# Kernel optimization log

Hardware: AMD Instinct MI355X
Metric: run time of the kernel (lower is better)

The kernel has to match this reference:

```python
import jax, jax.numpy as jnp
import numpy as np

N = 20000
E = 320000
D = 512
H = 512


def _gcn_norm(edge_index, num_nodes):
    # PyG GCNConv: add self-loops, then sym-normalize with in-degree of A+I
    src = jnp.concatenate([edge_index[0], jnp.arange(num_nodes)])
    dst = jnp.concatenate([edge_index[1], jnp.arange(num_nodes)])
    deg = jax.ops.segment_sum(jnp.ones_like(dst, dtype=jnp.float32), dst, num_segments=num_nodes)
    dinv = jnp.where(deg > 0, jax.lax.rsqrt(deg), 0.0)
    norm = dinv[src] * dinv[dst]  # [E+N]
    return src, dst, norm


def _gcn_layer(x, src, dst, norm, W, b, num_nodes):
    h = x @ W                          # [N, out]
    msg = h[src] * norm[:, None]       # gather + scale, [E+N, out]
    out = jax.ops.segment_sum(msg, dst, num_segments=num_nodes)  # scatter-add
    return out + b


def setup_inputs() -> dict:
    key = jax.random.key(0)
    ks = jax.random.split(key, 8)
    features = jax.random.normal(ks[0], (N, D), dtype=jnp.float32)
    edge_index = jax.random.randint(ks[1], (2, E), 0, N, dtype=jnp.int64)
    edge_attr = jax.random.normal(ks[2], (E, 1), dtype=jnp.float32)  # unused by GCNConv
    s1 = 1.0 / np.sqrt(D)
    s2 = 1.0 / np.sqrt(H)
    W1 = jax.random.uniform(ks[3], (D, H), dtype=jnp.float32, minval=-s1, maxval=s1)
    b1 = jnp.zeros((H,), dtype=jnp.float32)
    W2 = jax.random.uniform(ks[4], (H, H), dtype=jnp.float32, minval=-s2, maxval=s2)
    b2 = jnp.zeros((H,), dtype=jnp.float32)
    return {"features": features, "edge_index": edge_index, "edge_attr": edge_attr,
            "W1": W1, "b1": b1, "W2": W2, "b2": b2}


def reference(features, edge_index, edge_attr, W1, b1, W2, b2):
    src, dst, norm = _gcn_norm(edge_index, N)
    x = jax.nn.relu(_gcn_layer(features, src, dst, norm, W1, b1, N))
    x = jax.nn.relu(_gcn_layer(x, src, dst, norm, W2, b2, N))
    # global_max_pool over the single graph (batch = all zeros) -> [1, H]
    return jnp.max(x, axis=0, keepdims=True)
```

## Files before the change

kernel.cpp:

```cpp
#include <hip/hip_runtime.h>

#define N_NODES 20000
#define MP      20096
#define N_EDGES 320000
#define DIM     512
#define SCAN_BLOCKS 79
#define MAXP_BLOCKS 256
#define MAXP_ROWS   79

typedef _Float16 half8 __attribute__((ext_vector_type(8)));
typedef _Float16 half4v __attribute__((ext_vector_type(4)));
typedef float floatx4 __attribute__((ext_vector_type(4)));

#define GLD16(g, l) __builtin_amdgcn_global_load_lds( \
    (const __attribute__((address_space(1))) unsigned int*)(g), \
    (__attribute__((address_space(3))) unsigned int*)(l), 16, 0, 0)

__global__ void k_init(int* __restrict__ cnt, float* __restrict__ out) {
    int i = blockIdx.x * blockDim.x + threadIdx.x;
    if (i < N_NODES) cnt[i] = 0;
    if (i < DIM) out[i] = 0.f;
}

__global__ void k_count(const int* __restrict__ dst, int* __restrict__ cnt) {
    int e = blockIdx.x * blockDim.x + threadIdx.x;
    if (e < N_EDGES) atomicAdd(&cnt[dst[e]], 1);
}

__global__ __launch_bounds__(256) void k_scan_a(const int* __restrict__ cnt,
                                                int* __restrict__ bsum) {
    __shared__ int buf[256];
    int gi = blockIdx.x * 256 + threadIdx.x;
    buf[threadIdx.x] = (gi < N_NODES) ? cnt[gi] : 0;
    __syncthreads();
    for (int off = 128; off > 0; off >>= 1) {
        if (threadIdx.x < off) buf[threadIdx.x] += buf[threadIdx.x + off];
        __syncthreads();
    }
    if (threadIdx.x == 0) bsum[blockIdx.x] = buf[0];
}

__global__ __launch_bounds__(128) void k_scan_b(const int* __restrict__ bsum,
                                                int* __restrict__ bbase) {
    __shared__ int buf[128];
    int tid = threadIdx.x;
    int v = (tid < SCAN_BLOCKS) ? bsum[tid] : 0;
    buf[tid] = v;
    __syncthreads();
    for (int off = 1; off < 128; off <<= 1) {
        int t = (tid >= off) ? buf[tid - off] : 0;
        __syncthreads();
        buf[tid] += t;
        __syncthreads();
    }
    if (tid < SCAN_BLOCKS) bbase[tid] = buf[tid] - v;
}

__global__ __launch_bounds__(256) void k_scan_c(const int* __restrict__ cnt,
                                                const int* __restrict__ bbase,
                                                int* __restrict__ offs,
                                                int* __restrict__ cursor,
                                                float* __restrict__ dinv) {
    __shared__ int buf[256];
    int tid = threadIdx.x;
    int gi = blockIdx.x * 256 + tid;
    int v = (gi < N_NODES) ? cnt[gi] : 0;
    buf[tid] = v;
    __syncthreads();
    for (int off = 1; off < 256; off <<= 1) {
        int t = (tid >= off) ? buf[tid - off] : 0;
        __syncthreads();
        buf[tid] += t;
        __syncthreads();
    }
    int base = bbase[blockIdx.x];
    if (gi < N_NODES) {
        int incl = base + buf[tid];
        offs[gi + 1] = incl;
        cursor[gi] = incl - v;
        dinv[gi] = rsqrtf((float)v + 1.0f);
        if (gi == 0) offs[0] = 0;
    } else if (gi < MP) {
        dinv[gi] = 0.f;
    }
}

__global__ void k_fill(const int* __restrict__ src, const int* __restrict__ dst,
                       int* __restrict__ cursor, int* __restrict__ csr_src) {
    int e = blockIdx.x * blockDim.x + threadIdx.x;
    if (e < N_EDGES) {
        int d = dst[e];
        int pos = atomicAdd(&cursor[d], 1);
        csr_src[pos] = src[e];
    }
}

__global__ __launch_bounds__(256) void k_cvt_feat(const float* __restrict__ F,
                                                  _Float16* __restrict__ A) {
    int i = blockIdx.x * blockDim.x + threadIdx.x;
    int e = i * 4;
    int row = e >> 9;
    half4v o;
    if (row < N_NODES) {
        float4 v = *(const float4*)&F[e];
        o[0] = (_Float16)v.x; o[1] = (_Float16)v.y;
        o[2] = (_Float16)v.z; o[3] = (_Float16)v.w;
    } else {
        o[0] = o[1] = o[2] = o[3] = (_Float16)0.f;
    }
    *(half4v*)&A[e] = o;
}

__global__ __launch_bounds__(256) void k_cvt_w(const float* __restrict__ W1,
                                               const float* __restrict__ W2,
                                               _Float16* __restrict__ Wt1,
                                               _Float16* __restrict__ Wt2) {
    const float* W = blockIdx.z ? W2 : W1;
    _Float16* Wt = blockIdx.z ? Wt2 : Wt1;
    __shared__ float tile[32][33];
    int bx = blockIdx.x * 32, by = blockIdx.y * 32;
    int x = threadIdx.x & 31, y4 = (threadIdx.x >> 5) * 4;
#pragma unroll
    for (int r = 0; r < 4; ++r)
        tile[y4 + r][x] = W[(size_t)(by + y4 + r) * DIM + bx + x];
    __syncthreads();
#pragma unroll
    for (int r = 0; r < 4; ++r)
        Wt[(size_t)(bx + y4 + r) * DIM + by + x] = (_Float16)tile[x][y4 + r];
}

__global__ __launch_bounds__(256) void k_gemm_f16(const _Float16* __restrict__ A,
                                                  const _Float16* __restrict__ Bt,
                                                  const float* __restrict__ dinv,
                                                  _Float16* __restrict__ G) {
    __shared__ _Float16 As[128 * 32];
    __shared__ _Float16 Bs[128 * 32];

    int t = threadIdx.x;
    int w = t >> 6, lane = t & 63;
    int lm = lane & 15, quad = lane >> 4;
    int m0 = blockIdx.x * 128, n0 = blockIdx.y * 128;
    int wm = (w & 1) * 64, wn = (w >> 1) * 64;

    floatx4 acc[4][4];
#pragma unroll
    for (int i = 0; i < 4; ++i)
#pragma unroll
        for (int j = 0; j < 4; ++j) acc[i][j] = (floatx4){0.f, 0.f, 0.f, 0.f};

    for (int k0 = 0; k0 < DIM; k0 += 32) {
        __syncthreads();
#pragma unroll
        for (int i = 0; i < 2; ++i) {
            int s = i * 256 + t;
            int m = s >> 2, kk = (s & 3) * 8;
            GLD16(A + (size_t)(m0 + m) * DIM + k0 + kk, As + s * 8);
            GLD16(Bt + (size_t)(n0 + m) * DIM + k0 + kk, Bs + s * 8);
        }
        __syncthreads();

        half8 af[4], bf[4];
#pragma unroll
        for (int i = 0; i < 4; ++i)
            af[i] = *(const half8*)&As[(wm + i * 16 + lm) * 32 + quad * 8];
#pragma unroll
        for (int j = 0; j < 4; ++j)
            bf[j] = *(const half8*)&Bs[(wn + j * 16 + lm) * 32 + quad * 8];
#pragma unroll
        for (int i = 0; i < 4; ++i)
#pragma unroll
            for (int j = 0; j < 4; ++j)
                acc[i][j] = __builtin_amdgcn_mfma_f32_16x16x32_f16(af[i], bf[j], acc[i][j], 0, 0, 0);
    }

#pragma unroll
    for (int i = 0; i < 4; ++i)
#pragma unroll
        for (int r = 0; r < 4; ++r) {
            int row = m0 + wm + i * 16 + quad * 4 + r;
            float dd = dinv[row];
#pragma unroll
            for (int j = 0; j < 4; ++j) {
                int col = n0 + wn + j * 16 + lm;
                G[(size_t)row * DIM + col] = (_Float16)(dd * acc[i][j][r]);
            }
        }
}

__global__ __launch_bounds__(256) void k_agg(const _Float16* __restrict__ g,
                                             const float* __restrict__ dinv,
                                             const int* __restrict__ offs,
                                             const int* __restrict__ csr_src,
                                             const float* __restrict__ bias,
                                             _Float16* __restrict__ out, int nNodesOut) {
    int node = blockIdx.x * 4 + (threadIdx.x >> 6);
    int lane = threadIdx.x & 63;
    int f0 = lane * 8;
    if (node >= nNodesOut) return;
    if (node >= N_NODES) {
        half8 z;
#pragma unroll
        for (int i = 0; i < 8; ++i) z[i] = (_Float16)0.f;
        *(half8*)&out[(size_t)node * DIM + f0] = z;
        return;
    }
    float acc[8];
    half8 self = *(const half8*)&g[(size_t)node * DIM + f0];
#pragma unroll
    for (int i = 0; i < 8; ++i) acc[i] = (float)self[i];

    int beg = offs[node], end = offs[node + 1];
    int e = beg;
    for (; e + 8 <= end; e += 8) {
        int s0 = csr_src[e],     s1 = csr_src[e + 1], s2 = csr_src[e + 2], s3 = csr_src[e + 3];
        int s4 = csr_src[e + 4], s5 = csr_src[e + 5], s6 = csr_src[e + 6], s7 = csr_src[e + 7];
        half8 v0 = *(const half8*)&g[(size_t)s0 * DIM + f0];
        half8 v1 = *(const half8*)&g[(size_t)s1 * DIM + f0];
        half8 v2 = *(const half8*)&g[(size_t)s2 * DIM + f0];
        half8 v3 = *(const half8*)&g[(size_t)s3 * DIM + f0];
        half8 v4 = *(const half8*)&g[(size_t)s4 * DIM + f0];
        half8 v5 = *(const half8*)&g[(size_t)s5 * DIM + f0];
        half8 v6 = *(const half8*)&g[(size_t)s6 * DIM + f0];
        half8 v7 = *(const half8*)&g[(size_t)s7 * DIM + f0];
#pragma unroll
        for (int i = 0; i < 8; ++i)
            acc[i] += ((float)v0[i] + (float)v1[i]) + ((float)v2[i] + (float)v3[i]) +
                      ((float)v4[i] + (float)v5[i]) + ((float)v6[i] + (float)v7[i]);
    }
    for (; e + 4 <= end; e += 4) {
        int s0 = csr_src[e], s1 = csr_src[e + 1], s2 = csr_src[e + 2], s3 = csr_src[e + 3];
        half8 v0 = *(const half8*)&g[(size_t)s0 * DIM + f0];
        half8 v1 = *(const half8*)&g[(size_t)s1 * DIM + f0];
        half8 v2 = *(const half8*)&g[(size_t)s2 * DIM + f0];
        half8 v3 = *(const half8*)&g[(size_t)s3 * DIM + f0];
#pragma unroll
        for (int i = 0; i < 8; ++i)
            acc[i] += ((float)v0[i] + (float)v1[i]) + ((float)v2[i] + (float)v3[i]);
    }
    for (; e < end; ++e) {
        int s = csr_src[e];
        half8 v = *(const half8*)&g[(size_t)s * DIM + f0];
#pragma unroll
        for (int i = 0; i < 8; ++i) acc[i] += (float)v[i];
    }
    float dd = dinv[node];
    float4 b0 = *(const float4*)&bias[f0];
    float4 b1 = *(const float4*)&bias[f0 + 4];
    float bb[8] = {b0.x, b0.y, b0.z, b0.w, b1.x, b1.y, b1.z, b1.w};
    half8 o;
#pragma unroll
    for (int i = 0; i < 8; ++i) o[i] = (_Float16)fmaxf(fmaf(dd, acc[i], bb[i]), 0.f);
    *(half8*)&out[(size_t)node * DIM + f0] = o;
}

__global__ __launch_bounds__(256) void k_maxpool(const _Float16* __restrict__ x,
                                                 float* __restrict__ out) {
    __shared__ float lmax[4][DIM];
    int stream = threadIdx.x >> 6, lane = threadIdx.x & 63;
    int f0 = lane * 8;
    int r0 = blockIdx.x * MAXP_ROWS;
    int r1 = min(r0 + MAXP_ROWS, N_NODES);

    float m[8];
#pragma unroll
    for (int i = 0; i < 8; ++i) m[i] = 0.f;
    for (int r = r0 + stream; r < r1; r += 4) {
        half8 v = *(const half8*)&x[(size_t)r * DIM + f0];
#pragma unroll
        for (int i = 0; i < 8; ++i) m[i] = fmaxf(m[i], (float)v[i]);
    }
#pragma unroll
    for (int i = 0; i < 8; ++i) lmax[stream][f0 + i] = m[i];
    __syncthreads();
#pragma unroll
    for (int rep = 0; rep < 2; ++rep) {
        int f = rep * 256 + threadIdx.x;
        float v = fmaxf(fmaxf(lmax[0][f], lmax[1][f]), fmaxf(lmax[2][f], lmax[3][f]));
        atomicMax((int*)&out[f], __float_as_int(v));
    }
}

extern "C" void kernel_launch(void* const* d_in, const int* in_sizes, int n_in,
                              void* d_out, int out_size, void* d_ws, size_t ws_size,
                              hipStream_t stream) {
    const float* features = (const float*)d_in[0];
    const int*   ei       = (const int*)d_in[1];
    const float* W1       = (const float*)d_in[3];
    const float* b1       = (const float*)d_in[4];
    const float* W2       = (const float*)d_in[5];
    const float* b2       = (const float*)d_in[6];
    float* out = (float*)d_out;

    const int* src = ei;
    const int* dst = ei + N_EDGES;

    char* p = (char*)d_ws;
    auto alloc = [&](size_t bytes) { void* r = p; p += (bytes + 255) & ~(size_t)255; return r; };
    int*      cnt    = (int*)alloc(N_NODES * 4);
    int*      offs   = (int*)alloc((N_NODES + 1) * 4);
    int*      cursor = (int*)alloc(N_NODES * 4);
    float*    dinv   = (float*)alloc(MP * 4);
    int*      csr    = (int*)alloc(N_EDGES * 4);
    int*      bsum   = (int*)alloc(SCAN_BLOCKS * 4);
    int*      bbase  = (int*)alloc(SCAN_BLOCKS * 4);
    _Float16* fA  = (_Float16*)alloc((size_t)MP * DIM * 2);
    _Float16* Wt1 = (_Float16*)alloc((size_t)DIM * DIM * 2);
    _Float16* Wt2 = (_Float16*)alloc((size_t)DIM * DIM * 2);
    _Float16* gbuf = (_Float16*)alloc((size_t)MP * DIM * 2);
    _Float16* x1f  = (_Float16*)alloc((size_t)MP * DIM * 2);
    _Float16* x2h  = (_Float16*)alloc((size_t)MP * DIM * 2);

    k_init<<<SCAN_BLOCKS, 256, 0, stream>>>(cnt, out);
    k_count<<<(N_EDGES + 255) / 256, 256, 0, stream>>>(dst, cnt);
    k_scan_a<<<SCAN_BLOCKS, 256, 0, stream>>>(cnt, bsum);
    k_scan_b<<<1, 128, 0, stream>>>(bsum, bbase);
    k_scan_c<<<SCAN_BLOCKS, 256, 0, stream>>>(cnt, bbase, offs, cursor, dinv);
    k_fill<<<(N_EDGES + 255) / 256, 256, 0, stream>>>(src, dst, cursor, csr);

    k_cvt_feat<<<(MP * DIM / 4 + 255) / 256, 256, 0, stream>>>(features, fA);
    dim3 wgrd(16, 16, 2);
    k_cvt_w<<<wgrd, 256, 0, stream>>>(W1, W2, Wt1, Wt2);

    dim3 ggrd(MP / 128, DIM / 128);

    k_gemm_f16<<<ggrd, 256, 0, stream>>>(fA, Wt1, dinv, gbuf);
    k_agg<<<MP / 4, 256, 0, stream>>>(gbuf, dinv, offs, csr, b1, x1f, MP);

    k_gemm_f16<<<ggrd, 256, 0, stream>>>(x1f, Wt2, dinv, gbuf);
    k_agg<<<MP / 4, 256, 0, stream>>>(gbuf, dinv, offs, csr, b2, x2h, N_NODES);

    k_maxpool<<<MAXP_BLOCKS, 256, 0, stream>>>(x2h, out);
}
```

Baseline: 281.8 us.

## Split each node's aggregation across four waves and merge prep kernels

Measured after the change: 281.4 us. No clear change (-0.1%).

```diff
diff --git a/kernel.cpp b/kernel.cpp
--- a/kernel.cpp
+++ b/kernel.cpp
@@ -5,22 +5,20 @@
 #define N_EDGES 320000
 #define DIM     512
 #define SCAN_BLOCKS 79
+#define FILL_BLOCKS 1250
+#define CVT_BLOCKS  10048
+#define W_BLOCKS    512
 #define MAXP_BLOCKS 256
 #define MAXP_ROWS   79
 
 typedef _Float16 half8 __attribute__((ext_vector_type(8)));
 typedef _Float16 half4v __attribute__((ext_vector_type(4)));
+typedef _Float16 half2v __attribute__((ext_vector_type(2)));
 typedef float floatx4 __attribute__((ext_vector_type(4)));
 
 #define GLD16(g, l) __builtin_amdgcn_global_load_lds( \
     (const __attribute__((address_space(1))) unsigned int*)(g), \
     (__attribute__((address_space(3))) unsigned int*)(l), 16, 0, 0)
-
-__global__ void k_init(int* __restrict__ cnt, float* __restrict__ out) {
-    int i = blockIdx.x * blockDim.x + threadIdx.x;
-    if (i < N_NODES) cnt[i] = 0;
-    if (i < DIM) out[i] = 0.f;
-}
 
 __global__ void k_count(const int* __restrict__ dst, int* __restrict__ cnt) {
     int e = blockIdx.x * blockDim.x + threadIdx.x;
@@ -85,40 +83,45 @@
     }
 }
 
-__global__ void k_fill(const int* __restrict__ src, const int* __restrict__ dst,
-                       int* __restrict__ cursor, int* __restrict__ csr_src) {
-    int e = blockIdx.x * blockDim.x + threadIdx.x;
-    if (e < N_EDGES) {
+__global__ __launch_bounds__(256) void k_prep(const int* __restrict__ src,
+                                              const int* __restrict__ dst,
+                                              int* __restrict__ cursor,
+                                              int* __restrict__ csr_src,
+                                              const float* __restrict__ F,
+                                              _Float16* __restrict__ A,
+                                              const float* __restrict__ W1,
+                                              const float* __restrict__ W2,
+                                              _Float16* __restrict__ Wt1,
+                                              _Float16* __restrict__ Wt2) {
+    int b = blockIdx.x;
+    if (b < FILL_BLOCKS) {
+        int e = b * 256 + threadIdx.x;
         int d = dst[e];
         int pos = atomicAdd(&cursor[d], 1);
         csr_src[pos] = src[e];
-    }
-}
-
-__global__ __launch_bounds__(256) void k_cvt_feat(const float* __restrict__ F,
-                                                  _Float16* __restrict__ A) {
-    int i = blockIdx.x * blockDim.x + threadIdx.x;
-    int e = i * 4;
-    int row = e >> 9;
-    half4v o;
-    if (row < N_NODES) {
-        float4 v = *(const float4*)&F[e];
-        o[0] = (_Float16)v.x; o[1] = (_Float16)v.y;
-        o[2] = (_Float16)v.z; o[3] = (_Float16)v.w;
-    } else {
-        o[0] = o[1] = o[2] = o[3] = (_Float16)0.f;
-    }
-    *(half4v*)&A[e] = o;
-}
-
-__global__ __launch_bounds__(256) void k_cvt_w(const float* __restrict__ W1,
-                                               const float* __restrict__ W2,
-                                               _Float16* __restrict__ Wt1,
-                                               _Float16* __restrict__ Wt2) {
-    const float* W = blockIdx.z ? W2 : W1;
-    _Float16* Wt = blockIdx.z ? Wt2 : Wt1;
+        return;
+    }
+    if (b < FILL_BLOCKS + CVT_BLOCKS) {
+        int i = (b - FILL_BLOCKS) * 256 + threadIdx.x;
+        int e = i * 4;
+        int row = e >> 9;
+        half4v o;
+        if (row < N_NODES) {
+            float4 v = *(const float4*)&F[e];
+            o[0] = (_Float16)v.x; o[1] = (_Float16)v.y;
+            o[2] = (_Float16)v.z; o[3] = (_Float16)v.w;
+        } else {
+            o[0] = o[1] = o[2] = o[3] = (_Float16)0.f;
+        }
+        *(half4v*)&A[e] = o;
+        return;
+    }
+    int local = b - (FILL_BLOCKS + CVT_BLOCKS);
+    int z = local >> 8, t = local & 255;
+    const float* W = z ? W2 : W1;
+    _Float16* Wt = z ? Wt2 : Wt1;
     __shared__ float tile[32][33];
-    int bx = blockIdx.x * 32, by = blockIdx.y * 32;
+    int bx = (t & 15) * 32, by = (t >> 4) * 32;
     int x = threadIdx.x & 31, y4 = (threadIdx.x >> 5) * 4;
 #pragma unroll
     for (int r = 0; r < 4; ++r)
@@ -192,65 +195,56 @@
                                              const int* __restrict__ offs,
                                              const int* __restrict__ csr_src,
                                              const float* __restrict__ bias,
-                                             _Float16* __restrict__ out, int nNodesOut) {
-    int node = blockIdx.x * 4 + (threadIdx.x >> 6);
-    int lane = threadIdx.x & 63;
+                                             _Float16* __restrict__ out) {
+    int node = blockIdx.x;
+    if (node >= N_NODES) {
+        ((unsigned int*)&out[(size_t)node * DIM])[threadIdx.x] = 0u;
+        return;
+    }
+    __shared__ float part[4][DIM];
+    int w = threadIdx.x >> 6, lane = threadIdx.x & 63;
     int f0 = lane * 8;
-    if (node >= nNodesOut) return;
-    if (node >= N_NODES) {
-        half8 z;
-#pragma unroll
-        for (int i = 0; i < 8; ++i) z[i] = (_Float16)0.f;
-        *(half8*)&out[(size_t)node * DIM + f0] = z;
-        return;
-    }
+
     float acc[8];
-    half8 self = *(const half8*)&g[(size_t)node * DIM + f0];
-#pragma unroll
-    for (int i = 0; i < 8; ++i) acc[i] = (float)self[i];
+    if (w == 0) {
+        half8 self = *(const half8*)&g[(size_t)node * DIM + f0];
+#pragma unroll
+        for (int i = 0; i < 8; ++i) acc[i] = (float)self[i];
+    } else {
+#pragma unroll
+        for (int i = 0; i < 8; ++i) acc[i] = 0.f;
+    }
 
     int beg = offs[node], end = offs[node + 1];
-    int e = beg;
-    for (; e + 8 <= end; e += 8) {
-        int s0 = csr_src[e],     s1 = csr_src[e + 1], s2 = csr_src[e + 2], s3 = csr_src[e + 3];
-        int s4 = csr_src[e + 4], s5 = csr_src[e + 5], s6 = csr_src[e + 6], s7 = csr_src[e + 7];
+    int e = beg + w;
+    for (; e + 12 < end; e += 16) {
+        int s0 = csr_src[e], s1 = csr_src[e + 4], s2 = csr_src[e + 8], s3 = csr_src[e + 12];
         half8 v0 = *(const half8*)&g[(size_t)s0 * DIM + f0];
         half8 v1 = *(const half8*)&g[(size_t)s1 * DIM + f0];
         half8 v2 = *(const half8*)&g[(size_t)s2 * DIM + f0];
         half8 v3 = *(const half8*)&g[(size_t)s3 * DIM + f0];
-        half8 v4 = *(const half8*)&g[(size_t)s4 * DIM + f0];
-        half8 v5 = *(const half8*)&g[(size_t)s5 * DIM + f0];
-        half8 v6 = *(const half8*)&g[(size_t)s6 * DIM + f0];
-        half8 v7 = *(const half8*)&g[(size_t)s7 * DIM + f0];
-#pragma unroll
-        for (int i = 0; i < 8; ++i)
-            acc[i] += ((float)v0[i] + (float)v1[i]) + ((float)v2[i] + (float)v3[i]) +
-                      ((float)v4[i] + (float)v5[i]) + ((float)v6[i] + (float)v7[i]);
-    }
-    for (; e + 4 <= end; e += 4) {
-        int s0 = csr_src[e], s1 = csr_src[e + 1], s2 = csr_src[e + 2], s3 = csr_src[e + 3];
-        half8 v0 = *(const half8*)&g[(size_t)s0 * DIM + f0];
-        half8 v1 = *(const half8*)&g[(size_t)s1 * DIM + f0];
-        half8 v2 = *(const half8*)&g[(size_t)s2 * DIM + f0];
-        half8 v3 = *(const half8*)&g[(size_t)s3 * DIM + f0];
 #pragma unroll
         for (int i = 0; i < 8; ++i)
             acc[i] += ((float)v0[i] + (float)v1[i]) + ((float)v2[i] + (float)v3[i]);
     }
-    for (; e < end; ++e) {
+    for (; e < end; e += 4) {
         int s = csr_src[e];
         half8 v = *(const half8*)&g[(size_t)s * DIM + f0];
 #pragma unroll
         for (int i = 0; i < 8; ++i) acc[i] += (float)v[i];
     }
+#pragma unroll
+    for (int i = 0; i < 8; ++i) part[w][f0 + i] = acc[i];
+    __syncthreads();
+
+    int f = threadIdx.x * 2;
     float dd = dinv[node];
-    float4 b0 = *(const float4*)&bias[f0];
-    float4 b1 = *(const float4*)&bias[f0 + 4];
-    float bb[8] = {b0.x, b0.y, b0.z, b0.w, b1.x, b1.y, b1.z, b1.w};
-    half8 o;
-#pragma unroll
-    for (int i = 0; i < 8; ++i) o[i] = (_Float16)fmaxf(fmaf(dd, acc[i], bb[i]), 0.f);
-    *(half8*)&out[(size_t)node * DIM + f0] = o;
+    float s0 = part[0][f] + part[1][f] + part[2][f] + part[3][f];
+    float s1 = part[0][f + 1] + part[1][f + 1] + part[2][f + 1] + part[3][f + 1];
+    half2v o;
+    o[0] = (_Float16)fmaxf(fmaf(dd, s0, bias[f]), 0.f);
+    o[1] = (_Float16)fmaxf(fmaf(dd, s1, bias[f + 1]), 0.f);
+    *(half2v*)&out[(size_t)node * DIM + f] = o;
 }
 
 __global__ __launch_bounds__(256) void k_maxpool(const _Float16* __restrict__ x,
@@ -303,31 +297,31 @@
     int*      csr    = (int*)alloc(N_EDGES * 4);
     int*      bsum   = (int*)alloc(SCAN_BLOCKS * 4);
     int*      bbase  = (int*)alloc(SCAN_BLOCKS * 4);
-    _Float16* fA  = (_Float16*)alloc((size_t)MP * DIM * 2);
-    _Float16* Wt1 = (_Float16*)alloc((size_t)DIM * DIM * 2);
-    _Float16* Wt2 = (_Float16*)alloc((size_t)DIM * DIM * 2);
+    _Float16* fA   = (_Float16*)alloc((size_t)MP * DIM * 2);
+    _Float16* Wt1  = (_Float16*)alloc((size_t)DIM * DIM * 2);
+    _Float16* Wt2  = (_Float16*)alloc((size_t)DIM * DIM * 2);
     _Float16* gbuf = (_Float16*)alloc((size_t)MP * DIM * 2);
     _Float16* x1f  = (_Float16*)alloc((size_t)MP * DIM * 2);
     _Float16* x2h  = (_Float16*)alloc((size_t)MP * DIM * 2);
 
-    k_init<<<SCAN_BLOCKS, 256, 0, stream>>>(cnt, out);
-    k_count<<<(N_EDGES + 255) / 256, 256, 0, stream>>>(dst, cnt);
+    hipMemsetAsync(cnt, 0, N_NODES * 4, stream);
+    hipMemsetAsync(out, 0, DIM * 4, stream);
+
+    k_count<<<FILL_BLOCKS, 256, 0, stream>>>(dst, cnt);
     k_scan_a<<<SCAN_BLOCKS, 256, 0, stream>>>(cnt, bsum);
     k_scan_b<<<1, 128, 0, stream>>>(bsum, bbase);
     k_scan_c<<<SCAN_BLOCKS, 256, 0, stream>>>(cnt, bbase, offs, cursor, dinv);
-    k_fill<<<(N_EDGES + 255) / 256, 256, 0, stream>>>(src, dst, cursor, csr);
-
-    k_cvt_feat<<<(MP * DIM / 4 + 255) / 256, 256, 0, stream>>>(features, fA);
-    dim3 wgrd(16, 16, 2);
-    k_cvt_w<<<wgrd, 256, 0, stream>>>(W1, W2, Wt1, Wt2);
+
+    k_prep<<<FILL_BLOCKS + CVT_BLOCKS + W_BLOCKS, 256, 0, stream>>>(
+        src, dst, cursor, csr, features, fA, W1, W2, Wt1, Wt2);
 
     dim3 ggrd(MP / 128, DIM / 128);
 
     k_gemm_f16<<<ggrd, 256, 0, stream>>>(fA, Wt1, dinv, gbuf);
-    k_agg<<<MP / 4, 256, 0, stream>>>(gbuf, dinv, offs, csr, b1, x1f, MP);
+    k_agg<<<MP, 256, 0, stream>>>(gbuf, dinv, offs, csr, b1, x1f);
 
     k_gemm_f16<<<ggrd, 256, 0, stream>>>(x1f, Wt2, dinv, gbuf);
-    k_agg<<<MP / 4, 256, 0, stream>>>(gbuf, dinv, offs, csr, b2, x2h, N_NODES);
+    k_agg<<<N_NODES, 256, 0, stream>>>(gbuf, dinv, offs, csr, b2, x2h);
 
     k_maxpool<<<MAXP_BLOCKS, 256, 0, stream>>>(x2h, out);
 }
```
